# Performance work log

Measured on AMD Instinct MI355X. Metric: run time of the kernel, lower is better.

## Reference

```python
import jax, jax.numpy as jnp
import numpy as np

K = 1024
D = 256
BETA = 0.25
DECAY = 0.99
EPS = 1e-05


def setup_inputs() -> dict:
    key = jax.random.key(0)
    k1, k2, k3, k4 = jax.random.split(key, 4)
    z_e = jax.random.normal(k1, (32, 2048, D), dtype=jnp.float32)
    emb = jax.random.normal(k2, (K, D), dtype=jnp.float32)
    # module L2-normalizes the codebook rows at init
    emb = emb / jnp.linalg.norm(emb, axis=1, keepdims=True)
    cluster_size = jax.random.uniform(k3, (K,), dtype=jnp.float32)
    embed_avg = jax.random.normal(k4, (K, D), dtype=jnp.float32)
    return {"z_e": z_e, "embedding": emb, "cluster_size": cluster_size, "embed_avg": embed_avg}


def reference(z_e, embedding, cluster_size, embed_avg):
    B, T, d = z_e.shape
    z = z_e.reshape(-1, d)                                   # [N, D]
    # squared-distance matrix: ||z||^2 - 2 z E^T + ||e||^2   -> [N, K]
    z_sq = jnp.sum(z * z, axis=1, keepdims=True)
    e_sq = jnp.sum(embedding * embedding, axis=1)[None, :]
    dist = z_sq - 2.0 * (z @ embedding.T) + e_sq
    codes = jnp.argmin(dist, axis=1)                         # [N]
    z_q = embedding[codes].reshape(z_e.shape)                # gather + reshape

    # ---- EMA codebook update (training branch, no-grad in torch) ----
    # scatter-reduce instead of materializing the [N, K] one-hot
    cs_batch = jax.ops.segment_sum(jnp.ones_like(codes, dtype=z.dtype), codes, num_segments=K)
    embed_sum = jax.ops.segment_sum(z, codes, num_segments=K)          # [K, D]
    new_cluster_size = cluster_size * DECAY + cs_batch * (1.0 - DECAY)
    new_embed_avg = embed_avg * DECAY + embed_sum * (1.0 - DECAY)
    n = jnp.sum(new_cluster_size)
    cs_smoothed = (new_cluster_size + EPS) / (n + K * EPS) * n
    new_embedding = new_embed_avg / cs_smoothed[:, None]

    commit_loss = jnp.mean((z_e - z_q) ** 2)
    vq_loss = BETA * commit_loss
    z_q_st = z_e + (z_q - z_e)  # straight-through (identical values in fwd)
    return (z_q_st, vq_loss, codes.reshape(B, T), new_embedding, new_cluster_size, new_embed_avg)
```

## Files before the change

### kernel.cpp

```cpp
#include <hip/hip_runtime.h>


#define DDIM 256
#define DQ   64
#define KC   1024
#define NROW 65536
#define BM   128
#define BN   128
#define BD   32
#define LS   34
#define DECAYF 0.99f
#define OMDF   0.01f
#define BETAF  0.25f
#define EPSF   1e-5f

#define BMR  128
#define NIT  48

typedef _Float16 f16;
typedef _Float16 f16x8 __attribute__((ext_vector_type(8)));
typedef float    f32x4 __attribute__((ext_vector_type(4)));

__device__ __forceinline__ void gl_lds16(const f16* g, f16* l) {
    __builtin_amdgcn_global_load_lds(
        (const __attribute__((address_space(1))) void*)g,
        (__attribute__((address_space(3))) void*)l, 16, 0, 0);
}

__global__ __launch_bounds__(256) void vq_esq(const float* __restrict__ emb,
                                              float* __restrict__ esq_g)
{
    int k = blockIdx.x * 256 + threadIdx.x;
    const float4* ep = (const float4*)(emb + (size_t)k * DDIM);
    float s = 0.f;
    for (int q = 0; q < DQ; ++q) {
        float4 v = ep[q];
        s += v.x * v.x + v.y * v.y + v.z * v.z + v.w * v.w;
    }
    esq_g[k] = s;
}

__global__ __launch_bounds__(256) void vq_prep(const float* __restrict__ src,
                                               f16* __restrict__ dst,
                                               float* __restrict__ sq_g)
{
    int t   = blockIdx.x * 256 + threadIdx.x;
    int row = t >> 5;
    int c   = t & 31;
    const float4* sp = (const float4*)(src + (size_t)row * DDIM + c * 8);
    float4 v0 = sp[0], v1 = sp[1];
    float x[8] = {v0.x, v0.y, v0.z, v0.w, v1.x, v1.y, v1.z, v1.w};
    f16x8 h, l;
    float s = 0.f;
#pragma unroll
    for (int j = 0; j < 8; ++j) {
        float xs = x[j] * 128.0f;
        f16 hh = (f16)xs;
        h[j] = hh;
        l[j] = (f16)(xs - (float)hh);
        s += x[j] * x[j];
    }
    f16* rp = dst + (size_t)row * 512;
    *(f16x8*)(rp + c * 8)       = h;
    *(f16x8*)(rp + 256 + c * 8) = l;
    s += __shfl_xor(s, 1);
    s += __shfl_xor(s, 2);
    s += __shfl_xor(s, 4);
    s += __shfl_xor(s, 8);
    s += __shfl_xor(s, 16);
    if (c == 0) sq_g[row] = s;
}

__global__ __launch_bounds__(256) void vq_prep_e(const float* __restrict__ emb,
                                                 f16* __restrict__ ehl2,
                                                 float* __restrict__ esq_g)
{
    int t     = blockIdx.x * 256 + threadIdx.x;
    int c     = t >> 5;
    int chunk = t & 31;
    const float4* sp = (const float4*)(emb + (size_t)c * DDIM + chunk * 8);
    float4 v0 = sp[0], v1 = sp[1];
    float x[8] = {v0.x, v0.y, v0.z, v0.w, v1.x, v1.y, v1.z, v1.w};
    f16x8 h, l;
    float s = 0.f;
#pragma unroll
    for (int j = 0; j < 8; ++j) {
        float xs = x[j] * 128.0f;
        f16 hh = (f16)xs;
        h[j] = hh;
        l[j] = (f16)(xs - (float)hh);
        s += x[j] * x[j];
    }
    int kb = chunk >> 2, kg = chunk & 3;
    int cg = c >> 4;
    int lanep = kg * 16 + (c & 15);
    size_t idx = ((size_t)(kb * 64 + cg)) * 512 + lanep * 8;
    *(f16x8*)(ehl2 + idx)          = h;
    *(f16x8*)(ehl2 + 262144 + idx) = l;
    s += __shfl_xor(s, 1);
    s += __shfl_xor(s, 2);
    s += __shfl_xor(s, 4);
    s += __shfl_xor(s, 8);
    s += __shfl_xor(s, 16);
    if (chunk == 0) esq_g[c] = s;
}


#define FOLD(P) do {                                                        \
    _Pragma("unroll")                                                       \
    for (int i_ = 0; i_ < 4; ++i_) {                                        \
      _Pragma("unroll")                                                     \
      for (int t_ = 0; t_ < 4; ++t_) {                                      \
        int row_ = wr * 64 + i_ * 16 + kg * 4 + t_;                         \
        float zq2_ = zsq_s[row_];                                           \
        float bv_ = 3.4e38f; int bix_ = 0;                                  \
        _Pragma("unroll")                                                   \
        for (int j_ = 0; j_ < 8; ++j_) {                                    \
          int col_ = (P) * 512 + wc * 128 + j_ * 16 + c16;                  \
          float d_ = fmaf(acc[i_][j_][t_], -0x1p-13f, zq2_) + esq_s[col_];  \
          if (d_ < bv_) { bv_ = d_; bix_ = col_; }                          \
        }                                                                   \
        _Pragma("unroll")                                                   \
        for (int m_ = 1; m_ < 16; m_ <<= 1) {                               \
          float ov_ = __shfl_xor(bv_, m_);                                  \
          int   oi_ = __shfl_xor(bix_, m_);                                 \
          if (ov_ < bv_ || (ov_ == bv_ && oi_ < bix_)) { bv_ = ov_; bix_ = oi_; } \
        }                                                                   \
        if (c16 == 0) {                                                     \
          red_v2[row_ * 8 + (P) * 4 + wc] = bv_;                            \
          red_i2[row_ * 8 + (P) * 4 + wc] = bix_;                           \
        }                                                                   \
      }                                                                     \
    }                                                                       \
    _Pragma("unroll")                                                       \
    for (int i_ = 0; i_ < 4; ++i_)                                          \
      _Pragma("unroll")                                                     \
      for (int j_ = 0; j_ < 8; ++j_) acc[i_][j_] = zero4;                   \
} while (0)

#define BODY(IT, BC, BN_) do {                                              \
    asm volatile("s_waitcnt vmcnt(9)" ::: "memory");                        \
    __builtin_amdgcn_s_barrier();                                           \
    const f16* Ab_ = &Abuf[(IT) % 3][0];                                    \
    f16x8 af0 = *(const f16x8*)(Ab_ + ((wr4 + 0) * 64 + lane) * 8);         \
    f16x8 af1 = *(const f16x8*)(Ab_ + ((wr4 + 1) * 64 + lane) * 8);         \
    f16x8 af2 = *(const f16x8*)(Ab_ + ((wr4 + 2) * 64 + lane) * 8);         \
    f16x8 af3 = *(const f16x8*)(Ab_ + ((wr4 + 3) * 64 + lane) * 8);         \
    {   \
      int itn_ = (IT) + 1; if (itn_ > NIT - 1) itn_ = NIT - 1;              \
      int kbn_ = itn_ % 24; int pn_ = itn_ / 24;                            \
      int bpl_ = (kbn_ >= 8 && kbn_ < 16) ? 1 : 0;                          \
      const f16* bp_ = ehl2 + (((size_t)((bpl_ * 8 + (kbn_ & 7)) * 64       \
                        + pn_ * 32 + wc8)) << 9) + lane * 8;                \
      _Pragma("unroll")                                                     \
      for (int j_ = 0; j_ < 8; ++j_)                                        \
          BN_[j_] = *(const f16x8*)(bp_ + j_ * 512);                        \
    }                                                                       \
    {                  \
      int its_ = (IT) + 2;                                                  \
      int bs_ = its_ % 3;                                                   \
      if (its_ > NIT - 1) its_ = NIT - 1;                                   \
      int kbs_ = its_ % 24;                                                 \
      int aoff_ = ((kbs_ & 16) ? 256 : 0) + (kbs_ & 7) * 32;                \
      gl_lds16(astage + aoff_, &Abuf[bs_][0] + (size_t)tid * 8);            \
    }                                                                       \
    __builtin_amdgcn_s_setprio(1);                                          \
    _Pragma("unroll")                                                       \
    for (int j_ = 0; j_ < 8; ++j_) {                                        \
        acc[0][j_] = __builtin_amdgcn_mfma_f32_16x16x32_f16(af0, BC[j_], acc[0][j_], 0, 0, 0); \
        acc[1][j_] = __builtin_amdgcn_mfma_f32_16x16x32_f16(af1, BC[j_], acc[1][j_], 0, 0, 0); \
        acc[2][j_] = __builtin_amdgcn_mfma_f32_16x16x32_f16(af2, BC[j_], acc[2][j_], 0, 0, 0); \
        acc[3][j_] = __builtin_amdgcn_mfma_f32_16x16x32_f16(af3, BC[j_], acc[3][j_], 0, 0, 0); \
    }                                                                       \
    __builtin_amdgcn_s_setprio(0);                                          \
    if (((IT) % 24) == 23) { FOLD((IT) / 24); }                             \
} while (0)

__global__ __launch_bounds__(512) void vq_main_mfma(
    const float* __restrict__ z,
    const float* __restrict__ emb,
    const f16*  __restrict__ zhl,
    const f16*  __restrict__ ehl2,
    const float* __restrict__ esq_g,
    const float* __restrict__ zsq_g,
    float* __restrict__ out_zq,
    float* __restrict__ out_codes,
    float* __restrict__ loss_acc)
{
    __shared__ f16   Abuf[3][4096];
    __shared__ float esq_s[KC];
    __shared__ float zsq_s[BMR];
    __shared__ float red_v2[BMR * 8];
    __shared__ int   red_i2[BMR * 8];
    __shared__ int   codes_s[BMR];
    __shared__ float lred[512];

    const int tid  = threadIdx.x;
    const int row0 = blockIdx.x * BMR;
    const int wave = tid >> 6, lane = tid & 63;
    const int wr   = wave >> 2, wc = wave & 3;
    const int wr4  = wr * 4;
    const int wc8  = wc * 8;
    const int kg   = lane >> 4, c16 = lane & 15;

    { float2 v = ((const float2*)esq_g)[tid];
      *(float2*)(esq_s + tid * 2) = v; }
    if (tid < BMR) zsq_s[tid] = zsq_g[row0 + tid];

    const f16* astage = zhl + (size_t)(row0 + (tid >> 6) * 16 + (tid & 15)) * 512
                            + ((tid >> 4) & 3) * 8;

    f16x8 bA[8], bB[8];
    gl_lds16(astage + 0,  &Abuf[0][0] + (size_t)tid * 8);
    gl_lds16(astage + 32, &Abuf[1][0] + (size_t)tid * 8);
    {
        const f16* bp = ehl2 + ((size_t)wc8 << 9) + lane * 8;
#pragma unroll
        for (int j = 0; j < 8; ++j) bA[j] = *(const f16x8*)(bp + j * 512);
    }
    asm volatile("s_waitcnt lgkmcnt(0)" ::: "memory");

    f32x4 acc[4][8];
    const f32x4 zero4 = {0.f, 0.f, 0.f, 0.f};
#pragma unroll
    for (int i = 0; i < 4; ++i)
#pragma unroll
        for (int j = 0; j < 8; ++j) acc[i][j] = zero4;

#pragma unroll 1
    for (int it = 0; it < NIT; it += 2) {
        BODY(it,     bA, bB);
        BODY(it + 1, bB, bA);
    }

    __syncthreads();
    if (tid < BMR) {
        float bv = red_v2[tid * 8];
        int   bi = red_i2[tid * 8];
#pragma unroll
        for (int t = 1; t < 8; ++t) {
            float v  = red_v2[tid * 8 + t];
            int   ix = red_i2[tid * 8 + t];
            if (v < bv || (v == bv && ix < bi)) { bv = v; bi = ix; }
        }
        codes_s[tid] = bi;
        out_codes[row0 + tid] = (float)bi;
    }
    __syncthreads();

    float lp = 0.f;
#pragma unroll 1
    for (int r = wave; r < BMR; r += 8) {
        int code = codes_s[r];
        float4 e4 = *(const float4*)(emb + (size_t)code * DDIM + lane * 4);
        float4 z4 = *(const float4*)(z + (size_t)(row0 + r) * DDIM + lane * 4);
        float dx = e4.x - z4.x, dy = e4.y - z4.y, dz = e4.z - z4.z, dw = e4.w - z4.w;
        float4 o;
        o.x = z4.x + dx; o.y = z4.y + dy; o.z = z4.z + dz; o.w = z4.w + dw;
        *(float4*)(out_zq + (size_t)(row0 + r) * DDIM + lane * 4) = o;
        lp += dx * dx + dy * dy + dz * dz + dw * dw;
    }
    lred[tid] = lp;
    __syncthreads();
    for (int st = 256; st > 0; st >>= 1) {
        if (tid < st) lred[tid] += lred[tid + st];
        __syncthreads();
    }
    if (tid == 0) atomicAdd(loss_acc, lred[0]);
}

__global__ __launch_bounds__(256) void vq_main_f32(
    const float* __restrict__ z,
    const float* __restrict__ emb,
    const float* __restrict__ esq_g,
    float* __restrict__ out_zq,
    float* __restrict__ out_codes,
    float* __restrict__ loss_acc)
{
    __shared__ float zs[BM * LS];
    __shared__ float es[BN * LS];
    __shared__ float esq_s[KC];
    __shared__ float zsq_s[BM];
    float* red_v   = zs;
    int*   red_i   = (int*)(zs + 2048);
    int*   codes_s = (int*)es;
    float* lred    = es + 128;

    const int tid  = threadIdx.x;
    const int row0 = blockIdx.x * BM;
    const int trow = tid >> 4;
    const int tcol = tid & 15;

    {
        const float4* eg = (const float4*)esq_g;
        float4 v = eg[tid];
        *(float4*)(esq_s + tid * 4) = v;
    }
    if (tid < BM) {
        const float4* zp = (const float4*)(z + (size_t)(row0 + tid) * DDIM);
        float s = 0.f;
        for (int q = 0; q < DQ; ++q) {
            float4 v = zp[q];
            s += v.x * v.x + v.y * v.y + v.z * v.z + v.w * v.w;
        }
        zsq_s[tid] = s;
    }

    const int r0 = tid >> 3;
    const int q0 = tid & 7;
    const float* zp0 = z + (size_t)(row0 + r0) * DDIM + q0 * 4;
    const float* ep0 = emb + (size_t)r0 * DDIM + q0 * 4;
    const int ls0 = r0 * LS + q0 * 4;

    float4 pz[4], pe[4];
#pragma unroll
    for (int it = 0; it < 4; ++it) {
        pz[it] = *(const float4*)(zp0 + it * 32 * DDIM);
        pe[it] = *(const float4*)(ep0 + it * 32 * DDIM);
    }

    float runv[8];
    int   runi[8];
#pragma unroll
    for (int i = 0; i < 8; ++i) { runv[i] = 3.4e38f; runi[i] = 0; }

#pragma unroll 1
    for (int kt = 0; kt < KC / BN; ++kt) {
        float acc[8][8];
#pragma unroll
        for (int i = 0; i < 8; ++i)
#pragma unroll
            for (int j = 0; j < 8; ++j) acc[i][j] = 0.f;

#pragma unroll 1
        for (int dc = 0; dc < DDIM / BD; ++dc) {
            __syncthreads();
#pragma unroll
            for (int it = 0; it < 4; ++it) {
                int o = ls0 + it * 32 * LS;
                *(float2*)(zs + o)     = make_float2(pz[it].x, pz[it].y);
                *(float2*)(zs + o + 2) = make_float2(pz[it].z, pz[it].w);
                *(float2*)(es + o)     = make_float2(pe[it].x, pe[it].y);
                *(float2*)(es + o + 2) = make_float2(pe[it].z, pe[it].w);
            }
            __syncthreads();
            {
                int ndc = dc + 1, nkt = kt;
                if (ndc == DDIM / BD) { ndc = 0; ++nkt; }
                if (nkt < KC / BN) {
                    size_t zo = (size_t)ndc * BD;
                    size_t eo = (size_t)nkt * BN * DDIM + (size_t)ndc * BD;
#pragma unroll
                    for (int it = 0; it < 4; ++it) {
                        pz[it] = *(const float4*)(zp0 + it * 32 * DDIM + zo);
                        pe[it] = *(const float4*)(ep0 + it * 32 * DDIM + eo);
                    }
                }
            }
#pragma unroll
            for (int s = 0; s < BD / 2; ++s) {
                float2 a2[8], b2[8];
#pragma unroll
                for (int i = 0; i < 8; ++i)
                    a2[i] = *(const float2*)(zs + (trow + 16 * i) * LS + s * 2);
#pragma unroll
                for (int j = 0; j < 8; ++j)
                    b2[j] = *(const float2*)(es + (tcol + 16 * j) * LS + s * 2);
#pragma unroll
                for (int i = 0; i < 8; ++i)
#pragma unroll
                    for (int j = 0; j < 8; ++j)
                        acc[i][j] = fmaf(a2[i].y, b2[j].y,
                                     fmaf(a2[i].x, b2[j].x, acc[i][j]));
            }
        }
#pragma unroll
        for (int i = 0; i < 8; ++i) {
            float zq2 = zsq_s[trow + 16 * i];
#pragma unroll
            for (int j = 0; j < 8; ++j) {
                int col = kt * BN + tcol + 16 * j;
                float dist = zq2 - 2.f * acc[i][j] + esq_s[col];
                if (dist < runv[i]) { runv[i] = dist; runi[i] = col; }
            }
        }
    }

    __syncthreads();
#pragma unroll
    for (int i = 0; i < 8; ++i) {
        int lr = trow + 16 * i;
        red_v[lr * 16 + tcol] = runv[i];
        red_i[lr * 16 + tcol] = runi[i];
    }
    __syncthreads();
    if (tid < BM) {
        float bv = red_v[tid * 16];
        int   bi = red_i[tid * 16];
        for (int t = 1; t < 16; ++t) {
            float v  = red_v[tid * 16 + t];
            int   ix = red_i[tid * 16 + t];
            if (v < bv || (v == bv && ix < bi)) { bv = v; bi = ix; }
        }
        codes_s[tid] = bi;
        out_codes[row0 + tid] = (float)bi;
    }
    __syncthreads();

    const int wavf = tid >> 6;
    const int lanf = tid & 63;
    float lp = 0.f;
    for (int r = wavf; r < BM; r += 4) {
        int code = codes_s[r];
        float4 e4 = *(const float4*)(emb + (size_t)code * DDIM + lanf * 4);
        float4 z4 = *(const float4*)(z + (size_t)(row0 + r) * DDIM + lanf * 4);
        float dx = e4.x - z4.x, dy = e4.y - z4.y, dz = e4.z - z4.z, dw = e4.w - z4.w;
        float4 o;
        o.x = z4.x + dx; o.y = z4.y + dy; o.z = z4.z + dz; o.w = z4.w + dw;
        *(float4*)(out_zq + (size_t)(row0 + r) * DDIM + lanf * 4) = o;
        lp += dx * dx + dy * dy + dz * dz + dw * dw;
    }
    lred[tid] = lp;
    __syncthreads();
    for (int s = 128; s > 0; s >>= 1) {
        if (tid < s) lred[tid] += lred[tid + s];
        __syncthreads();
    }
    if (tid == 0) atomicAdd(loss_acc, lred[0]);
}

__global__ __launch_bounds__(256) void vq_scatter(
    const float* __restrict__ z,
    const float* __restrict__ codes_f,
    float* __restrict__ embed_sum,
    float* __restrict__ counts)
{
    __shared__ int list[1024];
    __shared__ int nmatch;
    const int k   = blockIdx.x;
    const int tid = threadIdx.x;

    float acc = 0.f;
    int total = 0;
    if (tid == 0) nmatch = 0;
    __syncthreads();

    for (int base = 0; base < NROW; base += 1024) {
        float4 c4 = *(const float4*)(codes_f + base + tid * 4);
        int i0 = base + tid * 4;
        if ((int)c4.x == k) { int p = atomicAdd(&nmatch, 1); list[p] = i0; }
        if ((int)c4.y == k) { int p = atomicAdd(&nmatch, 1); list[p] = i0 + 1; }
        if ((int)c4.z == k) { int p = atomicAdd(&nmatch, 1); list[p] = i0 + 2; }
        if ((int)c4.w == k) { int p = atomicAdd(&nmatch, 1); list[p] = i0 + 3; }
        __syncthreads();
        int nm = nmatch;
        for (int i = 0; i < nm; ++i)
            acc += z[(size_t)list[i] * DDIM + tid];
        total += nm;
        __syncthreads();
        if (tid == 0) nmatch = 0;
        __syncthreads();
    }
    embed_sum[(size_t)k * DDIM + tid] = acc;
    if (tid == 0) counts[k] = (float)total;
}

__global__ void vq_finalize(const float* __restrict__ cluster_size,
                            const float* __restrict__ counts,
                            const float* __restrict__ loss_acc,
                            float* __restrict__ out_ncs,
                            float* __restrict__ out_loss,
                            float* __restrict__ cs_sm,
                            float inv_ND)
{
    __shared__ float sred[KC];
    const int tid = threadIdx.x;
    float ncs = cluster_size[tid] * DECAYF + counts[tid] * OMDF;
    out_ncs[tid] = ncs;
    sred[tid] = ncs;
    __syncthreads();
    for (int s = KC / 2; s > 0; s >>= 1) {
        if (tid < s) sred[tid] += sred[tid + s];
        __syncthreads();
    }
    float n = sred[0];
    cs_sm[tid] = (ncs + EPSF) / (n + (float)KC * EPSF) * n;
    if (tid == 0) out_loss[0] = BETAF * loss_acc[0] * inv_ND;
}

__global__ void vq_embed(const float* __restrict__ embed_avg,
                         const float* __restrict__ embed_sum,
                         const float* __restrict__ cs_sm,
                         float* __restrict__ out_nea,
                         float* __restrict__ out_nemb)
{
    int idx = blockIdx.x * blockDim.x + threadIdx.x;
    int k = idx >> 6;
    float4 ea = ((const float4*)embed_avg)[idx];
    float4 s4 = ((const float4*)embed_sum)[idx];
    float4 nea;
    nea.x = ea.x * DECAYF + s4.x * OMDF;
    nea.y = ea.y * DECAYF + s4.y * OMDF;
    nea.z = ea.z * DECAYF + s4.z * OMDF;
    nea.w = ea.w * DECAYF + s4.w * OMDF;
    ((float4*)out_nea)[idx] = nea;
    float cs = cs_sm[k];
    float4 ne;
    ne.x = nea.x / cs; ne.y = nea.y / cs; ne.z = nea.z / cs; ne.w = nea.w / cs;
    ((float4*)out_nemb)[idx] = ne;
}

extern "C" void kernel_launch(void* const* d_in, const int* in_sizes, int n_in,
                              void* d_out, int out_size, void* d_ws, size_t ws_size,
                              hipStream_t stream) {
    const float* z            = (const float*)d_in[0];
    const float* emb          = (const float*)d_in[1];
    const float* cluster_size = (const float*)d_in[2];
    const float* embed_avg    = (const float*)d_in[3];

    const int ND = in_sizes[0];
    const int KD = in_sizes[1];
    const int K  = in_sizes[2];
    const int N  = ND / DDIM;

    float* out       = (float*)d_out;
    float* out_zq    = out;
    float* out_loss  = out + (size_t)ND;
    float* out_codes = out + (size_t)ND + 1;
    float* out_nemb  = out + (size_t)ND + 1 + N;
    float* out_ncs   = out_nemb + (size_t)KD;
    float* out_nea   = out_ncs + (size_t)K;

    float* ws        = (float*)d_ws;
    float* loss_acc  = ws;
    float* counts    = ws + 1;
    float* cs_sm     = counts + K;
    float* esq_g     = cs_sm + K;
    float* zsq_g     = esq_g + K;
    float* embed_sum = zsq_g + N;

    size_t base_floats = (size_t)1 + 3 * (size_t)K + (size_t)N + (size_t)KD;
    size_t f16_off = (base_floats * sizeof(float) + 255) & ~(size_t)255;
    size_t zbytes  = (size_t)N * 512 * sizeof(f16);
    size_t ebytes  = (size_t)2 * 262144 * sizeof(f16);
    bool mfma_ok   = ws_size >= f16_off + zbytes + ebytes;

    hipMemsetAsync(loss_acc, 0, sizeof(float), stream);
    if (mfma_ok) {
        f16* zhl  = (f16*)((char*)d_ws + f16_off);
        f16* ehl2 = (f16*)((char*)d_ws + f16_off + zbytes);
        vq_prep<<<(N * 32) / 256, 256, 0, stream>>>(z, zhl, zsq_g);
        vq_prep_e<<<(K * 32) / 256, 256, 0, stream>>>(emb, ehl2, esq_g);
        vq_main_mfma<<<N / BMR, 512, 0, stream>>>(
            z, emb, zhl, ehl2, esq_g, zsq_g, out_zq, out_codes, loss_acc);
    } else {
        vq_esq<<<K / 256, 256, 0, stream>>>(emb, esq_g);
        vq_main_f32<<<N / BM, 256, 0, stream>>>(z, emb, esq_g,
                                                out_zq, out_codes, loss_acc);
    }
    vq_scatter<<<K, 256, 0, stream>>>(z, out_codes, embed_sum, counts);
    vq_finalize<<<1, K, 0, stream>>>(cluster_size, counts, loss_acc,
                                     out_ncs, out_loss, cs_sm, 1.0f / (float)ND);
    vq_embed<<<KD / 1024, 256, 0, stream>>>(embed_avg, embed_sum, cs_sm,
                                            out_nea, out_nemb);
}
```

Before: 339.5 us.

## Double K-depth per MFMA iteration with swizzled A staging, split epilogue kernel

The main MFMA loop now stages 64 f16 K-columns of A per buffer (double-size LDS tiles, XOR-swizzled to avoid bank conflicts) and issues two MFMA sub-steps per iteration. This halves the iteration count and the number of barriers. The reduction arrays are padded to stride 9. The z_q gather and loss computation move out of the GEMM kernel into a separate epilogue kernel, which frees LDS and registers in the main kernel at the cost of an extra launch and a re-read of codes.

```diff
diff --git a/kernel.cpp b/kernel.cpp
--- a/kernel.cpp
+++ b/kernel.cpp
@@ -15,7 +15,7 @@
 #define EPSF   1e-5f
 
 #define BMR  128
-#define NIT  48
+#define NIT  24
 
 typedef _Float16 f16;
 typedef _Float16 f16x8 __attribute__((ext_vector_type(8)));
@@ -105,6 +105,39 @@
     if (chunk == 0) esq_g[c] = s;
 }
 
+
+#define ASTAGE(b_, s_) do {                                                 \
+    int off_ = (((s_) >= 8) ? 256 : 0) + ((s_) & 3) * 64;                   \
+    gl_lds16(asrc0 + off_, &Abuf[b_][0] + tid * 8);                         \
+    gl_lds16(asrc1 + off_, &Abuf[b_][0] + (tid + 512) * 8);                 \
+} while (0)
+
+#define BLOAD(dst_, it_, ks_) do {                                          \
+    int itc_ = (it_) > NIT - 1 ? NIT - 1 : (it_);                           \
+    int ps_ = itc_ / 12, sb_ = itc_ % 12;                                   \
+    int pl_ = (sb_ >= 4 && sb_ < 8) ? 1 : 0;                                \
+    int kb_ = (sb_ & 3) * 2 + (ks_);                                        \
+    const f16* bp_ = ehl2 + (((pl_ * 8 + kb_) * 64 + ps_ * 32 + wc * 8) << 9) \
+                   + lane * 8;                                              \
+    _Pragma("unroll")                                                       \
+    for (int j_ = 0; j_ < 8; ++j_) dst_[j_] = *(const f16x8*)(bp_ + j_ * 512); \
+} while (0)
+
+#define MM(bank_, Ab_, ks_) do {                                            \
+    f16x8 a0_ = *(const f16x8*)((Ab_) + aoff[0][ks_]);                      \
+    f16x8 a1_ = *(const f16x8*)((Ab_) + aoff[1][ks_]);                      \
+    f16x8 a2_ = *(const f16x8*)((Ab_) + aoff[2][ks_]);                      \
+    f16x8 a3_ = *(const f16x8*)((Ab_) + aoff[3][ks_]);                      \
+    __builtin_amdgcn_s_setprio(1);                                          \
+    _Pragma("unroll")                                                       \
+    for (int j_ = 0; j_ < 8; ++j_) {                                        \
+        acc[0][j_] = __builtin_amdgcn_mfma_f32_16x16x32_f16(a0_, bank_[j_], acc[0][j_], 0, 0, 0); \
+        acc[1][j_] = __builtin_amdgcn_mfma_f32_16x16x32_f16(a1_, bank_[j_], acc[1][j_], 0, 0, 0); \
+        acc[2][j_] = __builtin_amdgcn_mfma_f32_16x16x32_f16(a2_, bank_[j_], acc[2][j_], 0, 0, 0); \
+        acc[3][j_] = __builtin_amdgcn_mfma_f32_16x16x32_f16(a3_, bank_[j_], acc[3][j_], 0, 0, 0); \
+    }                                                                       \
+    __builtin_amdgcn_s_setprio(0);                                          \
+} while (0)
 
 #define FOLD(P) do {                                                        \
     _Pragma("unroll")                                                       \
@@ -127,8 +160,8 @@
           if (ov_ < bv_ || (ov_ == bv_ && oi_ < bix_)) { bv_ = ov_; bix_ = oi_; } \
         }                                                                   \
         if (c16 == 0) {                                                     \
-          red_v2[row_ * 8 + (P) * 4 + wc] = bv_;                            \
-          red_i2[row_ * 8 + (P) * 4 + wc] = bix_;                           \
+          red_v[row_ * 9 + (P) * 4 + wc] = bv_;                             \
+          red_i[row_ * 9 + (P) * 4 + wc] = bix_;                            \
         }                                                                   \
       }                                                                     \
     }                                                                       \
@@ -138,87 +171,48 @@
       for (int j_ = 0; j_ < 8; ++j_) acc[i_][j_] = zero4;                   \
 } while (0)
 
-#define BODY(IT, BC, BN_) do {                                              \
-    asm volatile("s_waitcnt vmcnt(9)" ::: "memory");                        \
-    __builtin_amdgcn_s_barrier();                                           \
-    const f16* Ab_ = &Abuf[(IT) % 3][0];                                    \
-    f16x8 af0 = *(const f16x8*)(Ab_ + ((wr4 + 0) * 64 + lane) * 8);         \
-    f16x8 af1 = *(const f16x8*)(Ab_ + ((wr4 + 1) * 64 + lane) * 8);         \
-    f16x8 af2 = *(const f16x8*)(Ab_ + ((wr4 + 2) * 64 + lane) * 8);         \
-    f16x8 af3 = *(const f16x8*)(Ab_ + ((wr4 + 3) * 64 + lane) * 8);         \
-    {   \
-      int itn_ = (IT) + 1; if (itn_ > NIT - 1) itn_ = NIT - 1;              \
-      int kbn_ = itn_ % 24; int pn_ = itn_ / 24;                            \
-      int bpl_ = (kbn_ >= 8 && kbn_ < 16) ? 1 : 0;                          \
-      const f16* bp_ = ehl2 + (((size_t)((bpl_ * 8 + (kbn_ & 7)) * 64       \
-                        + pn_ * 32 + wc8)) << 9) + lane * 8;                \
-      _Pragma("unroll")                                                     \
-      for (int j_ = 0; j_ < 8; ++j_)                                        \
-          BN_[j_] = *(const f16x8*)(bp_ + j_ * 512);                        \
-    }                                                                       \
-    {                  \
-      int its_ = (IT) + 2;                                                  \
-      int bs_ = its_ % 3;                                                   \
-      if (its_ > NIT - 1) its_ = NIT - 1;                                   \
-      int kbs_ = its_ % 24;                                                 \
-      int aoff_ = ((kbs_ & 16) ? 256 : 0) + (kbs_ & 7) * 32;                \
-      gl_lds16(astage + aoff_, &Abuf[bs_][0] + (size_t)tid * 8);            \
-    }                                                                       \
-    __builtin_amdgcn_s_setprio(1);                                          \
-    _Pragma("unroll")                                                       \
-    for (int j_ = 0; j_ < 8; ++j_) {                                        \
-        acc[0][j_] = __builtin_amdgcn_mfma_f32_16x16x32_f16(af0, BC[j_], acc[0][j_], 0, 0, 0); \
-        acc[1][j_] = __builtin_amdgcn_mfma_f32_16x16x32_f16(af1, BC[j_], acc[1][j_], 0, 0, 0); \
-        acc[2][j_] = __builtin_amdgcn_mfma_f32_16x16x32_f16(af2, BC[j_], acc[2][j_], 0, 0, 0); \
-        acc[3][j_] = __builtin_amdgcn_mfma_f32_16x16x32_f16(af3, BC[j_], acc[3][j_], 0, 0, 0); \
-    }                                                                       \
-    __builtin_amdgcn_s_setprio(0);                                          \
-    if (((IT) % 24) == 23) { FOLD((IT) / 24); }                             \
-} while (0)
-
 __global__ __launch_bounds__(512) void vq_main_mfma(
-    const float* __restrict__ z,
-    const float* __restrict__ emb,
     const f16*  __restrict__ zhl,
     const f16*  __restrict__ ehl2,
     const float* __restrict__ esq_g,
     const float* __restrict__ zsq_g,
-    float* __restrict__ out_zq,
-    float* __restrict__ out_codes,
-    float* __restrict__ loss_acc)
-{
-    __shared__ f16   Abuf[3][4096];
+    float* __restrict__ out_codes)
+{
+    __shared__ f16   Abuf[3][8192];
     __shared__ float esq_s[KC];
     __shared__ float zsq_s[BMR];
-    __shared__ float red_v2[BMR * 8];
-    __shared__ int   red_i2[BMR * 8];
-    __shared__ int   codes_s[BMR];
-    __shared__ float lred[512];
+    __shared__ float red_v[BMR * 9];
+    __shared__ int   red_i[BMR * 9];
 
     const int tid  = threadIdx.x;
     const int row0 = blockIdx.x * BMR;
     const int wave = tid >> 6, lane = tid & 63;
     const int wr   = wave >> 2, wc = wave & 3;
-    const int wr4  = wr * 4;
-    const int wc8  = wc * 8;
     const int kg   = lane >> 4, c16 = lane & 15;
 
     { float2 v = ((const float2*)esq_g)[tid];
       *(float2*)(esq_s + tid * 2) = v; }
     if (tid < BMR) zsq_s[tid] = zsq_g[row0 + tid];
 
-    const f16* astage = zhl + (size_t)(row0 + (tid >> 6) * 16 + (tid & 15)) * 512
-                            + ((tid >> 4) & 3) * 8;
-
-    f16x8 bA[8], bB[8];
-    gl_lds16(astage + 0,  &Abuf[0][0] + (size_t)tid * 8);
-    gl_lds16(astage + 32, &Abuf[1][0] + (size_t)tid * 8);
-    {
-        const f16* bp = ehl2 + ((size_t)wc8 << 9) + lane * 8;
-#pragma unroll
-        for (int j = 0; j < 8; ++j) bA[j] = *(const f16x8*)(bp + j * 512);
-    }
+    const int ar = tid >> 3, ach = tid & 7;
+    const f16* asrc0 = zhl + (size_t)(row0 + ar) * 512 + (ach ^ (ar & 7)) * 8;
+    const f16* asrc1 = asrc0 + (size_t)64 * 512;
+
+    int aoff[4][2];
+#pragma unroll
+    for (int i = 0; i < 4; ++i)
+#pragma unroll
+        for (int ks = 0; ks < 2; ++ks)
+            aoff[i][ks] = (wr * 64 + i * 16 + c16) * 64
+                        + (((ks * 4 + kg) ^ (c16 & 7)) * 8);
+
+    f16x8 b0[8], b1[8];
+    ASTAGE(0, 0);
+    ASTAGE(1, 1);
+    BLOAD(b0, 0, 0);
     asm volatile("s_waitcnt lgkmcnt(0)" ::: "memory");
+    asm volatile("s_waitcnt vmcnt(10)" ::: "memory");
+    __builtin_amdgcn_s_barrier();
 
     f32x4 acc[4][8];
     const f32x4 zero4 = {0.f, 0.f, 0.f, 0.f};
@@ -228,29 +222,56 @@
         for (int j = 0; j < 8; ++j) acc[i][j] = zero4;
 
 #pragma unroll 1
-    for (int it = 0; it < NIT; it += 2) {
-        BODY(it,     bA, bB);
-        BODY(it + 1, bB, bA);
+    for (int it = 0; it < NIT; ++it) {
+        const f16* Ab = &Abuf[it % 3][0];
+        BLOAD(b1, it, 1);
+        MM(b0, Ab, 0);
+        BLOAD(b0, it + 1, 0);
+        {
+            int its = it + 2;
+            int bd  = its % 3;
+            int ssv = (its > NIT - 1 ? NIT - 1 : its) % 12;
+            ASTAGE(bd, ssv);
+        }
+        MM(b1, Ab, 1);
+        if ((it % 12) == 11) { FOLD(it / 12); }
+        asm volatile("s_waitcnt vmcnt(18)" ::: "memory");
+        __builtin_amdgcn_s_barrier();
     }
 
     __syncthreads();
     if (tid < BMR) {
-        float bv = red_v2[tid * 8];
-        int   bi = red_i2[tid * 8];
+        float bv = red_v[tid * 9];
+        int   bi = red_i[tid * 9];
 #pragma unroll
         for (int t = 1; t < 8; ++t) {
-            float v  = red_v2[tid * 8 + t];
-            int   ix = red_i2[tid * 8 + t];
+            float v  = red_v[tid * 9 + t];
+            int   ix = red_i[tid * 9 + t];
             if (v < bv || (v == bv && ix < bi)) { bv = v; bi = ix; }
         }
-        codes_s[tid] = bi;
         out_codes[row0 + tid] = (float)bi;
     }
+}
+
+__global__ __launch_bounds__(256) void vq_epi(
+    const float* __restrict__ z,
+    const float* __restrict__ emb,
+    const float* __restrict__ codes_f,
+    float* __restrict__ out_zq,
+    float* __restrict__ loss_acc)
+{
+    __shared__ int   codes_s[64];
+    __shared__ float lred[256];
+    const int tid  = threadIdx.x;
+    const int row0 = blockIdx.x * 64;
+    const int wave = tid >> 6, lane = tid & 63;
+
+    if (tid < 64) codes_s[tid] = (int)codes_f[row0 + tid];
     __syncthreads();
 
     float lp = 0.f;
 #pragma unroll 1
-    for (int r = wave; r < BMR; r += 8) {
+    for (int r = wave; r < 64; r += 4) {
         int code = codes_s[r];
         float4 e4 = *(const float4*)(emb + (size_t)code * DDIM + lane * 4);
         float4 z4 = *(const float4*)(z + (size_t)(row0 + r) * DDIM + lane * 4);
@@ -262,8 +283,8 @@
     }
     lred[tid] = lp;
     __syncthreads();
-    for (int st = 256; st > 0; st >>= 1) {
-        if (tid < st) lred[tid] += lred[tid + st];
+    for (int s = 128; s > 0; s >>= 1) {
+        if (tid < s) lred[tid] += lred[tid + s];
         __syncthreads();
     }
     if (tid == 0) atomicAdd(loss_acc, lred[0]);
@@ -552,7 +573,8 @@
         vq_prep<<<(N * 32) / 256, 256, 0, stream>>>(z, zhl, zsq_g);
         vq_prep_e<<<(K * 32) / 256, 256, 0, stream>>>(emb, ehl2, esq_g);
         vq_main_mfma<<<N / BMR, 512, 0, stream>>>(
-            z, emb, zhl, ehl2, esq_g, zsq_g, out_zq, out_codes, loss_acc);
+            zhl, ehl2, esq_g, zsq_g, out_codes);
+        vq_epi<<<N / 64, 256, 0, stream>>>(z, emb, out_codes, out_zq, loss_acc);
     } else {
         vq_esq<<<K / 256, 256, 0, stream>>>(emb, esq_g);
         vq_main_f32<<<N / BM, 256, 0, stream>>>(z, emb, esq_g,
```

Measured after the change: 353.4 us. +4.1%, slower.
